# Performance work log

Hardware: AMD Instinct MI355X
Metric: run time of the kernel (lower is better)

The kernel has to match this reference:

```python
import jax, jax.numpy as jnp
import numpy as np

NUM_NODES = 200000
MAX_DEG = 32
BATCH = 8192
MEM_DIM = 128
TIME_DIM = 64
TAU = 0.1
W_S, L_S = 10, 3
W_L, L_L = 5, 10
W_T, L_T = 5, 8
NEG = -1e30


def setup_inputs() -> dict:
    key = jax.random.key(0)
    ks = jax.random.split(key, 8)
    return {
        "source_nodes": jax.random.randint(ks[0], (BATCH,), 0, NUM_NODES),
        # source times in [0.5, 1.0) so most neighbors (times in [0,1)) are temporally valid
        "current_times": jax.random.uniform(ks[1], (BATCH,), jnp.float32, 0.5, 1.0),
        "neighbor_ids": jax.random.randint(ks[2], (NUM_NODES, MAX_DEG), 0, NUM_NODES),
        "neighbor_times": jax.random.uniform(ks[3], (NUM_NODES, MAX_DEG)),
        "memory_states": jax.random.normal(ks[4], (NUM_NODES, MEM_DIM)),
        "restart_w": jax.random.normal(ks[5], (MEM_DIM + TIME_DIM,)) * 0.05,
        "restart_b": jnp.zeros(()),
        "time_w": jax.random.normal(ks[6], (TIME_DIM,)),
        "time_b": jax.random.normal(ks[7], (TIME_DIM,)),
    }


def _pack(first, rest, B, W, L):
    # first: [B*W], rest: [L-1, B*W] -> [B, W, L]
    x = jnp.concatenate([first[None], rest], 0)  # [L, B*W]
    return x.T.reshape(B, W, L)


def _plain_walks(key, src, t0, nb_ids, nb_ts, num_walks, length):
    """Temporal-biased walks (Eq. 7): P(u,t'|v,t) = softmax(t'/tau) over neighbors with t' < t."""
    B = src.shape[0]
    n0 = jnp.repeat(src, num_walks)                      # [B*W]
    t0r = jnp.repeat(t0, num_walks)

    def step(carry, k):
        cur_n, cur_t, alive = carry
        ni = nb_ids[cur_n]                               # [BW, D] gather
        nt = nb_ts[cur_n]
        valid = nt < cur_t[:, None]
        has = jnp.any(valid, axis=-1)
        logits = jnp.where(valid, nt / TAU, NEG)         # softmax shift by t_max handled by categorical
        idx = jax.random.categorical(k, logits)          # [BW]
        nn = jnp.take_along_axis(ni, idx[:, None], 1)[:, 0]
        ntm = jnp.take_along_axis(nt, idx[:, None], 1)[:, 0]
        alive = alive & has
        cur_n = jnp.where(alive, nn, cur_n)
        cur_t = jnp.where(alive, ntm, cur_t)
        outs = (jnp.where(alive, nn, 0),
                jnp.where(alive, ntm, 0.0),
                alive.astype(jnp.float32))
        return (cur_n, cur_t, alive), outs

    keys = jax.random.split(key, length - 1)
    init = (n0, t0r, jnp.ones(n0.shape, bool))
    _, (ns, ts, ms) = jax.lax.scan(step, init, keys)
    nodes = _pack(n0, ns, B, num_walks, length)
    times = _pack(t0r, ts, B, num_walks, length)
    masks = _pack(jnp.ones_like(t0r), ms, B, num_walks, length)
    return nodes, times, masks


def _tawr_walks(key, src, t0, nb_ids, nb_ts, memory_states,
                restart_w, restart_b, time_w, time_b, num_walks, length):
    """Temporal anonymous walks with learnable restart rho = sigmoid(w^T [m_u || Phi(t)] + b)."""
    B = src.shape[0]
    n0 = jnp.repeat(src, num_walks)
    t0r = jnp.repeat(t0, num_walks)

    def step(carry, k):
        cur_n, cur_t, alive = carry
        k1, k2 = jax.random.split(k)
        # restart probability from memory state + time encoding Phi(t) = cos(t*w + b)
        phi = jnp.cos(cur_t[:, None] * time_w[None, :] + time_b[None, :])   # [BW, T]
        mem = memory_states[cur_n]                                           # [BW, M]
        feat = jnp.concatenate([mem, phi], axis=-1)
        rho = jax.nn.sigmoid(feat @ restart_w + restart_b)                   # [BW]
        restart = jax.random.uniform(k1, rho.shape) < rho
        # temporal-biased neighbor sampling
        ni = nb_ids[cur_n]
        nt = nb_ts[cur_n]
        valid = nt < cur_t[:, None]
        has = jnp.any(valid, axis=-1)
        logits = jnp.where(valid, nt / TAU, NEG)
        idx = jax.random.categorical(k2, logits)
        nn = jnp.take_along_axis(ni, idx[:, None], 1)[:, 0]
        ntm = jnp.take_along_axis(nt, idx[:, None], 1)[:, 0]
        # restart overrides neighbor step and keeps the walk alive
        nn = jnp.where(restart, n0, nn)
        ntm = jnp.where(restart, t0r, ntm)
        alive = alive & (restart | has)
        cur_n = jnp.where(alive, nn, cur_n)
        cur_t = jnp.where(alive, ntm, cur_t)
        m = alive.astype(jnp.float32)
        outs = (jnp.where(alive, nn, 0),
                jnp.where(alive, ntm, 0.0),
                m,
                (restart & alive).astype(jnp.float32),
                rho * m)
        return (cur_n, cur_t, alive), outs

    keys = jax.random.split(key, length - 1)
    init = (n0, t0r, jnp.ones(n0.shape, bool))
    _, (ns, ts, ms, rs, rhos) = jax.lax.scan(step, init, keys)
    z = jnp.zeros_like(t0r)
    nodes = _pack(n0, ns, B, num_walks, length)
    times = _pack(t0r, ts, B, num_walks, length)
    masks = _pack(jnp.ones_like(t0r), ms, B, num_walks, length)
    rflag = _pack(z, rs, B, num_walks, length)
    rho_o = _pack(z, rhos, B, num_walks, length)
    return nodes, times, masks, rflag, rho_o


def reference(source_nodes, current_times, neighbor_ids, neighbor_times,
              memory_states, restart_w, restart_b, time_w, time_b):
    key = jax.random.key(42)
    k1, k2, k3 = jax.random.split(key, 3)
    short = _plain_walks(k1, source_nodes, current_times, neighbor_ids, neighbor_times, W_S, L_S)
    longw = _plain_walks(k2, source_nodes, current_times, neighbor_ids, neighbor_times, W_L, L_L)
    tawr = _tawr_walks(k3, source_nodes, current_times, neighbor_ids, neighbor_times,
                       memory_states, restart_w, restart_b, time_w, time_b, W_T, L_T)
    return short + longw + tawr
```

## Files before the change

kernel.cpp:

```cpp
#include <hip/hip_runtime.h>
#include <stdint.h>
#include <math.h>


namespace {

constexpr int kB   = 8192;
constexpr int kWS  = 10, kLS = 3;
constexpr int kWL  = 5,  kLL = 10;
constexpr int kWT  = 5,  kLT = 8;
constexpr int kBWS = kB * kWS;
constexpr int kBWL = kB * kWL;
constexpr int kBWT = kB * kWT;

constexpr int O_SN = 0;
constexpr int O_ST = O_SN + kBWS * kLS;
constexpr int O_SM = O_ST + kBWS * kLS;
constexpr int O_LN = O_SM + kBWS * kLS;
constexpr int O_LT = O_LN + kBWL * kLL;
constexpr int O_LM = O_LT + kBWL * kLL;
constexpr int O_TN = O_LM + kBWL * kLL;
constexpr int O_TT = O_TN + kBWT * kLT;
constexpr int O_TM = O_TT + kBWT * kLT;
constexpr int O_TR = O_TM + kBWT * kLT;
constexpr int O_TQ = O_TR + kBWT * kLT;

struct Keys {
  uint32_t sk[kLS - 1][2];
  uint32_t lk[kLL - 1][2];
  uint32_t tu[kLT - 1][2];
  uint32_t tc[kLT - 1][2];
};

constexpr int kSlotStride = 68;

}

__host__ __device__ static inline void tf2x32(uint32_t k0, uint32_t k1,
                                              uint32_t x0, uint32_t x1,
                                              uint32_t& o0, uint32_t& o1) {
  uint32_t ks2 = k0 ^ k1 ^ 0x1BD11BDAu;
#define TFR(r) { x0 += x1; x1 = (x1 << (r)) | (x1 >> (32 - (r))); x1 ^= x0; }
  x0 += k0; x1 += k1;
  TFR(13) TFR(15) TFR(26) TFR(6)
  x0 += k1;  x1 += ks2 + 1u;
  TFR(17) TFR(29) TFR(16) TFR(24)
  x0 += ks2; x1 += k0 + 2u;
  TFR(13) TFR(15) TFR(26) TFR(6)
  x0 += k0;  x1 += k1 + 3u;
  TFR(17) TFR(29) TFR(16) TFR(24)
  x0 += k1;  x1 += ks2 + 4u;
  TFR(13) TFR(15) TFR(26) TFR(6)
  x0 += ks2; x1 += k0 + 5u;
#undef TFR
  o0 = x0; o1 = x1;
}

__device__ __forceinline__ uint32_t rbits32(uint32_t k0, uint32_t k1, uint32_t j) {
  uint32_t a, b;
  tf2x32(k0, k1, 0u, j, a, b);
  return a ^ b;
}

__device__ __forceinline__ float bits_to_u01(uint32_t bits) {
  return __uint_as_float((bits >> 9) | 0x3f800000u) - 1.0f;
}

__device__ __forceinline__ float gumbel_of(uint32_t k0, uint32_t k1, uint32_t j) {
  float u = bits_to_u01(rbits32(k0, k1, j));
  if (u == 0.0f) u = 1.17549435e-38f;
  return -logf(-logf(u));
}

struct Cat4 { int idx; float bt; bool has; };

__device__ __forceinline__ Cat4 categorical_g4(uint32_t k0, uint32_t k1,
                                               uint32_t j0,
                                               const float* __restrict__ row_t,
                                               float t, int r) {
  const float4* row4 = (const float4*)row_t;
  float4 v0 = row4[2 * r];
  float4 v1 = row4[2 * r + 1];
  float nv[8] = {v0.x, v0.y, v0.z, v0.w, v1.x, v1.y, v1.z, v1.w};
  float best = -INFINITY;
  int bidx = 0;
  float bbt = 0.0f;
#pragma unroll
  for (int e = 0; e < 8; ++e) {
    int d = 8 * r + e;
    float ntd = nv[e];
    bool valid = ntd < t;
    float g = gumbel_of(k0, k1, j0 + (uint32_t)d);
    float logit = valid ? __fdiv_rn(ntd, 0.1f) : -1e30f;
    float v = __fadd_rn(g, logit);
    if (v > best) { best = v; bidx = d; bbt = ntd; }
  }
#pragma unroll
  for (int m = 1; m <= 2; m <<= 1) {
    float ov = __shfl_xor(best, m);
    int   oi = __shfl_xor(bidx, m);
    float ob = __shfl_xor(bbt, m);
    if (ov > best || (ov == best && oi < bidx)) { best = ov; bidx = oi; bbt = ob; }
  }
  Cat4 c; c.idx = bidx; c.bt = bbt; c.has = best > -1e29f;
  return c;
}

template <int W, int L>
__device__ void plain_walk_g4(int bw, int r, const uint32_t keys[][2],
                              const int* __restrict__ src, const float* __restrict__ ct,
                              const int* __restrict__ nbi, const float* __restrict__ nbt,
                              float* __restrict__ on, float* __restrict__ ot,
                              float* __restrict__ om) {
  int b = bw / W;
  int cur = src[b];
  float t = ct[b];
  int obase = bw * L;
  if (r == 0) { on[obase] = (float)cur; ot[obase] = t; }
  else if (r == 1) { om[obase] = 1.0f; }
  bool alive = true;
  for (int s = 0; s < L - 1; ++s) {
    float wn = 0.0f, wt = 0.0f, wm = 0.0f;
    if (alive) {
      Cat4 c = categorical_g4(keys[s][0], keys[s][1], (uint32_t)bw * 32u,
                              nbt + (size_t)cur * 32, t, r);
      if (c.has) {
        cur = nbi[(size_t)cur * 32 + c.idx];
        t = c.bt;
        wn = (float)cur; wt = t; wm = 1.0f;
      } else {
        alive = false;
      }
    }
    int o = obase + s + 1;
    if (r == 0) on[o] = wn;
    else if (r == 1) ot[o] = wt;
    else if (r == 2) om[o] = wm;
  }
}

__global__ __launch_bounds__(256) void plain_kernel(
    const int* __restrict__ src, const float* __restrict__ ct,
    const int* __restrict__ nbi, const float* __restrict__ nbt,
    float* __restrict__ out, Keys K) {
  int tid = blockIdx.x * blockDim.x + threadIdx.x;
  int gid = tid >> 2;
  int r = tid & 3;
  if (gid < kBWL) {
    plain_walk_g4<kWL, kLL>(gid, r, K.lk, src, ct, nbi, nbt,
                            out + O_LN, out + O_LT, out + O_LM);
  } else {
    plain_walk_g4<kWS, kLS>(gid - kBWL, r, K.sk, src, ct, nbi, nbt,
                            out + O_SN, out + O_ST, out + O_SM);
  }
}

__device__ void tawr_g4(int bw, int r, float* __restrict__ slot, const Keys& K,
                        const int* __restrict__ src, const float* __restrict__ ct,
                        const int* __restrict__ nbi, const float* __restrict__ nbt,
                        const float* __restrict__ mem, const float* __restrict__ rw,
                        const float* __restrict__ rb, const float* __restrict__ tw,
                        const float* __restrict__ tb,
                        float* __restrict__ on, float* __restrict__ ot,
                        float* __restrict__ om, float* __restrict__ orf,
                        float* __restrict__ orh) {
  int b = bw / kWT;
  int n0 = src[b];
  float t0 = ct[b];
  float rbv = rb[0];
  int cur = n0;
  float t = t0;
  int obase = bw * kLT;
  if (r == 0) { on[obase] = (float)n0; ot[obase] = t0; }
  else if (r == 1) { om[obase] = 1.0f; orf[obase] = 0.0f; }
  else if (r == 2) { orh[obase] = 0.0f; }
  bool alive = true;

  const float4* rw4 = (const float4*)rw;
  const float4* tw4 = (const float4*)tw;
  const float4* tb4 = (const float4*)tb;

  for (int s = 0; s < kLT - 1; ++s) {
    float wn = 0.0f, wt = 0.0f, wm = 0.0f, wr = 0.0f, wq = 0.0f;
    if (alive) {
      const float4* mrow = (const float4*)(mem + (size_t)cur * 128);
      float acc = 0.0f;
#pragma unroll
      for (int ph = 0; ph < 2; ++ph) {
#pragma unroll
        for (int q = 0; q < 4; ++q) {
          int f4 = 16 * ph + 4 * r + q;
          float4 a = mrow[f4];
          float4 w = rw4[f4];
          float4 p;
          p.x = __fmul_rn(a.x, w.x); p.y = __fmul_rn(a.y, w.y);
          p.z = __fmul_rn(a.z, w.z); p.w = __fmul_rn(a.w, w.w);
          *(float4*)(slot + 16 * r + 4 * q) = p;
        }
        asm volatile("" ::: "memory");
#pragma unroll
        for (int q = 0; q < 16; ++q) {
          float4 p = *(const float4*)(slot + 4 * q);
          acc = __fadd_rn(acc, p.x); acc = __fadd_rn(acc, p.y);
          acc = __fadd_rn(acc, p.z); acc = __fadd_rn(acc, p.w);
        }
        asm volatile("" ::: "memory");
      }
#pragma unroll
      for (int q = 0; q < 4; ++q) {
        int f4 = 4 * r + q;
        float4 w = tw4[f4];
        float4 bb = tb4[f4];
        float4 rwp = rw4[32 + f4];
        float4 p;
        p.x = __fmul_rn(cosf(__fadd_rn(__fmul_rn(t, w.x), bb.x)), rwp.x);
        p.y = __fmul_rn(cosf(__fadd_rn(__fmul_rn(t, w.y), bb.y)), rwp.y);
        p.z = __fmul_rn(cosf(__fadd_rn(__fmul_rn(t, w.z), bb.z)), rwp.z);
        p.w = __fmul_rn(cosf(__fadd_rn(__fmul_rn(t, w.w), bb.w)), rwp.w);
        *(float4*)(slot + 16 * r + 4 * q) = p;
      }
      asm volatile("" ::: "memory");
#pragma unroll
      for (int q = 0; q < 16; ++q) {
        float4 p = *(const float4*)(slot + 4 * q);
        acc = __fadd_rn(acc, p.x); acc = __fadd_rn(acc, p.y);
        acc = __fadd_rn(acc, p.z); acc = __fadd_rn(acc, p.w);
      }
      asm volatile("" ::: "memory");

      float z = __fadd_rn(acc, rbv);
      float rho = __fdiv_rn(1.0f, __fadd_rn(1.0f, expf(-z)));
      float u = bits_to_u01(rbits32(K.tu[s][0], K.tu[s][1], (uint32_t)bw));
      bool restart = u < rho;

      bool has = false;
      int nn = 0;
      float ntm = 0.0f;
      if (!restart) {
        Cat4 c = categorical_g4(K.tc[s][0], K.tc[s][1], (uint32_t)bw * 32u,
                                nbt + (size_t)cur * 32, t, r);
        has = c.has;
        if (has) {
          nn = nbi[(size_t)cur * 32 + c.idx];
          ntm = c.bt;
        }
      } else {
        nn = n0;
        ntm = t0;
      }

      if (restart || has) {
        cur = nn; t = ntm;
        wn = (float)nn; wt = ntm; wm = 1.0f;
        wr = restart ? 1.0f : 0.0f;
        wq = rho;
      } else {
        alive = false;
      }
    }
    int o = obase + s + 1;
    if (r == 0) { on[o] = wn; ot[o] = wt; }
    else if (r == 1) { om[o] = wm; orf[o] = wr; }
    else if (r == 2) { orh[o] = wq; }
  }
}

__global__ __launch_bounds__(256) void tawr_kernel(
    const int* __restrict__ src, const float* __restrict__ ct,
    const int* __restrict__ nbi, const float* __restrict__ nbt,
    const float* __restrict__ mem, const float* __restrict__ rw,
    const float* __restrict__ rb, const float* __restrict__ tw,
    const float* __restrict__ tb, float* __restrict__ out, Keys K) {
  __shared__ float plds[64 * kSlotStride];
  int tid = blockIdx.x * blockDim.x + threadIdx.x;
  int gid = tid >> 2;
  int r = tid & 3;
  int ws = threadIdx.x >> 2;
  tawr_g4(gid, r, plds + ws * kSlotStride, K, src, ct, nbi, nbt, mem, rw, rb,
          tw, tb, out + O_TN, out + O_TT, out + O_TM, out + O_TR, out + O_TQ);
}

extern "C" void kernel_launch(void* const* d_in, const int* in_sizes, int n_in,
                              void* d_out, int out_size, void* d_ws, size_t ws_size,
                              hipStream_t stream) {
  (void)in_sizes; (void)n_in; (void)out_size; (void)d_ws; (void)ws_size;

  const int*   src = (const int*)d_in[0];
  const float* ct  = (const float*)d_in[1];
  const int*   nbi = (const int*)d_in[2];
  const float* nbt = (const float*)d_in[3];
  const float* mem = (const float*)d_in[4];
  const float* rw  = (const float*)d_in[5];
  const float* rb  = (const float*)d_in[6];
  const float* tw  = (const float*)d_in[7];
  const float* tb  = (const float*)d_in[8];
  float* out = (float*)d_out;

  Keys K;
  uint32_t k1[2], k2[2], k3[2];
  tf2x32(0u, 42u, 0u, 0u, k1[0], k1[1]);
  tf2x32(0u, 42u, 0u, 1u, k2[0], k2[1]);
  tf2x32(0u, 42u, 0u, 2u, k3[0], k3[1]);
  for (uint32_t s = 0; s < kLS - 1; ++s)
    tf2x32(k1[0], k1[1], 0u, s, K.sk[s][0], K.sk[s][1]);
  for (uint32_t s = 0; s < kLL - 1; ++s)
    tf2x32(k2[0], k2[1], 0u, s, K.lk[s][0], K.lk[s][1]);
  for (uint32_t s = 0; s < kLT - 1; ++s) {
    uint32_t ks[2];
    tf2x32(k3[0], k3[1], 0u, s, ks[0], ks[1]);
    tf2x32(ks[0], ks[1], 0u, 0u, K.tu[s][0], K.tu[s][1]);
    tf2x32(ks[0], ks[1], 0u, 1u, K.tc[s][0], K.tc[s][1]);
  }

  tawr_kernel<<<dim3(640), dim3(256), 0, stream>>>(src, ct, nbi, nbt, mem, rw,
                                                   rb, tw, tb, out, K);
  plain_kernel<<<dim3(1920), dim3(256), 0, stream>>>(src, ct, nbi, nbt, out, K);
}
```

Baseline: 328.9 us.

## Fuse TAWR and plain walk kernels into one interleaved launch, prefetch neighbor times

The TAWR and plain walk kernels are merged into a single launch. Blocks are interleaved one TAWR block to three plain blocks, so the compute-heavy restart walks and the latency-bound plain walks share the machine and the second launch is removed. In the TAWR step, the neighbor-time row is loaded alongside the memory row and the categorical sample is computed unconditionally before the restart decision, so the gather latency overlaps the dot-product work. This spends extra RNG and categorical work on steps that end in a restart.

```diff
diff --git a/kernel.cpp b/kernel.cpp
--- a/kernel.cpp
+++ b/kernel.cpp
@@ -74,13 +74,9 @@
 
 struct Cat4 { int idx; float bt; bool has; };
 
-__device__ __forceinline__ Cat4 categorical_g4(uint32_t k0, uint32_t k1,
-                                               uint32_t j0,
-                                               const float* __restrict__ row_t,
-                                               float t, int r) {
-  const float4* row4 = (const float4*)row_t;
-  float4 v0 = row4[2 * r];
-  float4 v1 = row4[2 * r + 1];
+__device__ __forceinline__ Cat4 categorical_g4v(uint32_t k0, uint32_t k1,
+                                                uint32_t j0, float4 v0,
+                                                float4 v1, float t, int r) {
   float nv[8] = {v0.x, v0.y, v0.z, v0.w, v1.x, v1.y, v1.z, v1.w};
   float best = -INFINITY;
   int bidx = 0;
@@ -122,8 +118,11 @@
   for (int s = 0; s < L - 1; ++s) {
     float wn = 0.0f, wt = 0.0f, wm = 0.0f;
     if (alive) {
-      Cat4 c = categorical_g4(keys[s][0], keys[s][1], (uint32_t)bw * 32u,
-                              nbt + (size_t)cur * 32, t, r);
+      const float4* row4 = (const float4*)(nbt + (size_t)cur * 32);
+      float4 v0 = row4[2 * r];
+      float4 v1 = row4[2 * r + 1];
+      Cat4 c = categorical_g4v(keys[s][0], keys[s][1], (uint32_t)bw * 32u,
+                               v0, v1, t, r);
       if (c.has) {
         cur = nbi[(size_t)cur * 32 + c.idx];
         t = c.bt;
@@ -136,22 +135,6 @@
     if (r == 0) on[o] = wn;
     else if (r == 1) ot[o] = wt;
     else if (r == 2) om[o] = wm;
-  }
-}
-
-__global__ __launch_bounds__(256) void plain_kernel(
-    const int* __restrict__ src, const float* __restrict__ ct,
-    const int* __restrict__ nbi, const float* __restrict__ nbt,
-    float* __restrict__ out, Keys K) {
-  int tid = blockIdx.x * blockDim.x + threadIdx.x;
-  int gid = tid >> 2;
-  int r = tid & 3;
-  if (gid < kBWL) {
-    plain_walk_g4<kWL, kLL>(gid, r, K.lk, src, ct, nbi, nbt,
-                            out + O_LN, out + O_LT, out + O_LM);
-  } else {
-    plain_walk_g4<kWS, kLS>(gid - kBWL, r, K.sk, src, ct, nbi, nbt,
-                            out + O_SN, out + O_ST, out + O_SM);
   }
 }
 
@@ -183,7 +166,11 @@
   for (int s = 0; s < kLT - 1; ++s) {
     float wn = 0.0f, wt = 0.0f, wm = 0.0f, wr = 0.0f, wq = 0.0f;
     if (alive) {
+      const float4* row4 = (const float4*)(nbt + (size_t)cur * 32);
+      float4 nv0 = row4[2 * r];
+      float4 nv1 = row4[2 * r + 1];
       const float4* mrow = (const float4*)(mem + (size_t)cur * 128);
+
       float acc = 0.0f;
 #pragma unroll
       for (int ph = 0; ph < 2; ++ph) {
@@ -230,26 +217,23 @@
 
       float z = __fadd_rn(acc, rbv);
       float rho = __fdiv_rn(1.0f, __fadd_rn(1.0f, expf(-z)));
+
+      Cat4 c = categorical_g4v(K.tc[s][0], K.tc[s][1], (uint32_t)bw * 32u,
+                               nv0, nv1, t, r);
+
       float u = bits_to_u01(rbits32(K.tu[s][0], K.tu[s][1], (uint32_t)bw));
       bool restart = u < rho;
 
-      bool has = false;
-      int nn = 0;
-      float ntm = 0.0f;
-      if (!restart) {
-        Cat4 c = categorical_g4(K.tc[s][0], K.tc[s][1], (uint32_t)bw * 32u,
-                                nbt + (size_t)cur * 32, t, r);
-        has = c.has;
-        if (has) {
-          nn = nbi[(size_t)cur * 32 + c.idx];
-          ntm = c.bt;
-        }
+      int nn; float ntm; bool keep;
+      if (restart) {
+        nn = n0; ntm = t0; keep = true;
       } else {
-        nn = n0;
-        ntm = t0;
-      }
-
-      if (restart || has) {
+        keep = c.has;
+        nn = keep ? nbi[(size_t)cur * 32 + c.idx] : 0;
+        ntm = c.bt;
+      }
+
+      if (keep) {
         cur = nn; t = ntm;
         wn = (float)nn; wt = ntm; wm = 1.0f;
         wr = restart ? 1.0f : 0.0f;
@@ -265,19 +249,36 @@
   }
 }
 
-__global__ __launch_bounds__(256) void tawr_kernel(
+__global__ __launch_bounds__(256) void walks_kernel(
     const int* __restrict__ src, const float* __restrict__ ct,
     const int* __restrict__ nbi, const float* __restrict__ nbt,
     const float* __restrict__ mem, const float* __restrict__ rw,
     const float* __restrict__ rb, const float* __restrict__ tw,
     const float* __restrict__ tb, float* __restrict__ out, Keys K) {
   __shared__ float plds[64 * kSlotStride];
-  int tid = blockIdx.x * blockDim.x + threadIdx.x;
-  int gid = tid >> 2;
-  int r = tid & 3;
-  int ws = threadIdx.x >> 2;
-  tawr_g4(gid, r, plds + ws * kSlotStride, K, src, ct, nbi, nbt, mem, rw, rb,
-          tw, tb, out + O_TN, out + O_TT, out + O_TM, out + O_TR, out + O_TQ);
+  int bid = blockIdx.x;
+  int q = bid >> 2;
+  int rr = bid & 3;
+  if (rr == 0) {
+    int tid = q * 256 + (int)threadIdx.x;
+    int gid = tid >> 2;
+    int r = tid & 3;
+    tawr_g4(gid, r, plds + (threadIdx.x >> 2) * kSlotStride, K, src, ct, nbi,
+            nbt, mem, rw, rb, tw, tb, out + O_TN, out + O_TT, out + O_TM,
+            out + O_TR, out + O_TQ);
+  } else {
+    int pbid = q * 3 + (rr - 1);
+    int tid = pbid * 256 + (int)threadIdx.x;
+    int gid = tid >> 2;
+    int r = tid & 3;
+    if (gid < kBWL) {
+      plain_walk_g4<kWL, kLL>(gid, r, K.lk, src, ct, nbi, nbt,
+                              out + O_LN, out + O_LT, out + O_LM);
+    } else {
+      plain_walk_g4<kWS, kLS>(gid - kBWL, r, K.sk, src, ct, nbi, nbt,
+                              out + O_SN, out + O_ST, out + O_SM);
+    }
+  }
 }
 
 extern "C" void kernel_launch(void* const* d_in, const int* in_sizes, int n_in,
@@ -312,7 +313,6 @@
     tf2x32(ks[0], ks[1], 0u, 1u, K.tc[s][0], K.tc[s][1]);
   }
 
-  tawr_kernel<<<dim3(640), dim3(256), 0, stream>>>(src, ct, nbi, nbt, mem, rw,
-                                                   rb, tw, tb, out, K);
-  plain_kernel<<<dim3(1920), dim3(256), 0, stream>>>(src, ct, nbi, nbt, out, K);
-}
+  walks_kernel<<<dim3(2560), dim3(256), 0, stream>>>(src, ct, nbi, nbt, mem,
+                                                     rw, rb, tw, tb, out, K);
+}
```

Result: slower. 440.4 us (+33.9%).
